# Kernel tuning notes

Hardware: AMD Instinct MI355X
Metric: run time of the kernel (lower is better)

The kernel has to match this reference:

```python
import jax, jax.numpy as jnp
import numpy as np

N_NODES = 50000
N_EDGES = 500000
N_GRAPHS = 64
IN_DIM = 64
HID = 128
N_LAYERS = 2
BN_EPS = 1e-5


def setup_inputs() -> dict:
    key = jax.random.key(0)
    ks = jax.random.split(key, 12)
    x = jax.random.normal(ks[0], (N_NODES, IN_DIM), dtype=jnp.float32)
    edge_index = jax.random.randint(ks[1], (2, N_EDGES), 0, N_NODES, dtype=jnp.int64)
    batch = jnp.sort(jax.random.randint(ks[2], (N_NODES,), 0, N_GRAPHS, dtype=jnp.int64))
    s = 0.05
    W_enc = jax.random.normal(ks[3], (IN_DIM, HID), dtype=jnp.float32) * s
    b_enc = jnp.zeros((HID,), dtype=jnp.float32)
    Wc = jax.random.normal(ks[4], (N_LAYERS, HID, HID), dtype=jnp.float32) * s
    bc = jnp.zeros((N_LAYERS, HID), dtype=jnp.float32)
    gamma = jnp.ones((N_LAYERS, HID), dtype=jnp.float32)
    beta = jnp.zeros((N_LAYERS, HID), dtype=jnp.float32)
    MID = HID // 2
    W1 = jax.random.normal(ks[5], (HID, MID), dtype=jnp.float32) * s
    b1 = jnp.zeros((MID,), dtype=jnp.float32)
    W2 = jax.random.normal(ks[6], (MID, 1), dtype=jnp.float32) * s
    b2 = jnp.zeros((1,), dtype=jnp.float32)
    return {"x": x, "edge_index": edge_index, "batch": batch,
            "W_enc": W_enc, "b_enc": b_enc, "Wc": Wc, "bc": bc,
            "gamma": gamma, "beta": beta, "W1": W1, "b1": b1,
            "W2": W2, "b2": b2}


def _gcn_conv(h, src, dst, norm, W, b, n_nodes):
    # h: [N, HID]; src/dst: [E+N] (self-loops included); norm: [E+N]
    h = h @ W                                   # [N, HID]
    msg = h[src] * norm[:, None]                # gather + normalize
    out = jax.ops.segment_sum(msg, dst, num_segments=n_nodes)  # scatter-add
    return out + b


def _batch_norm(h, g, b):
    mu = jnp.mean(h, axis=0)
    var = jnp.var(h, axis=0)
    return (h - mu) * jax.lax.rsqrt(var + BN_EPS) * g + b


def reference(x, edge_index, batch, W_enc, b_enc, Wc, bc, gamma, beta, W1, b1, W2, b2):
    n = x.shape[0]
    loop = jnp.arange(n, dtype=edge_index.dtype)
    src = jnp.concatenate([edge_index[0], loop])   # [E+N]
    dst = jnp.concatenate([edge_index[1], loop])
    # symmetric GCN normalization with self-loops: deg over target index
    deg = jax.ops.segment_sum(jnp.ones_like(dst, dtype=x.dtype), dst, num_segments=n)
    dinv = jax.lax.rsqrt(deg)                      # deg >= 1 due to self-loops
    norm = dinv[src] * dinv[dst]                   # [E+N]

    h = x @ W_enc + b_enc                          # node encoder
    for l in range(Wc.shape[0]):
        h = _gcn_conv(h, src, dst, norm, Wc[l], bc[l], n)
        h = _batch_norm(h, gamma[l], beta[l])
        h = jax.nn.relu(h)                         # dropout inactive (eval)

    # global mean pool over graphs
    pooled = jax.ops.segment_sum(h, batch, num_segments=N_GRAPHS)
    counts = jax.ops.segment_sum(jnp.ones((n,), dtype=h.dtype), batch, num_segments=N_GRAPHS)
    pooled = pooled / jnp.maximum(counts, 1.0)[:, None]

    z = jax.nn.relu(pooled @ W1 + b1)
    out = jax.nn.sigmoid(z @ W2 + b2)              # [B, 1]
    return out.squeeze(-1)                          # [B]
```

## Files before the change

kernel.cpp:

```cpp
#include <hip/hip_runtime.h>
#include <hip/hip_bf16.h>
#include <hip/hip_fp16.h>
#include <math.h>


typedef _Float16 f16x8 __attribute__((ext_vector_type(8)));
typedef float f32x4 __attribute__((ext_vector_type(4)));

__device__ inline unsigned pack2(float a, float b) {
  union { __half2 h; unsigned u; } p;
  p.h = __floats2half2_rn(a, b);
  return p.u;
}
__device__ inline float2 unpack2(unsigned u) {
  union { unsigned u; __half2 h; } p;
  p.u = u;
  return __half22float2(p.h);
}

__global__ __launch_bounds__(256) void k_setup(
    int* __restrict__ deg, float* __restrict__ pooled,
    float* __restrict__ bnstat, int statTotal, int N, int nbN,
    const float* __restrict__ W_enc, const float* __restrict__ b_enc,
    const float* __restrict__ Wc, unsigned short* __restrict__ MT,
    float* __restrict__ bfold, int NL,
    const float* __restrict__ Wc1, unsigned short* __restrict__ WT1,
    const int* __restrict__ batch, int* __restrict__ gstart) {
  int b = blockIdx.x;
  if (b < nbN) {
    int i = b * 256 + threadIdx.x;
    if (i < N) deg[i] = 1;
    if (i < 64 * 128) pooled[i] = 0.f;
    if (i < statTotal) bnstat[i] = 0.f;
    return;
  }
  b -= nbN;
  if (b < 65) {
    if (threadIdx.x < 128) {
      int n = threadIdx.x;
      int k = b;
      const float* arow = (k < 64) ? (W_enc + (size_t)k * 128) : b_enc;
      float acc = 0.f;
      for (int j = 0; j < 128; j++)
        acc = fmaf(arow[j], Wc[(size_t)j * 128 + n], acc);
      if (k < 64) ((__half*)MT)[(size_t)n * 64 + k] = __float2half(acc);
      else bfold[n] = acc;
    }
    return;
  }
  b -= 65;
  if (b < 64) {
    if (NL > 1) {
      int i = b * 256 + threadIdx.x;
      int n = i & 127, k = i >> 7;
      ((__half*)WT1)[(size_t)n * 128 + k] = __float2half(Wc1[i]);
    }
    return;
  }
  int g = threadIdx.x;
  if (g <= 64) {
    int lo = 0, hi = N;
    while (lo < hi) {
      int mid = (lo + hi) >> 1;
      if (batch[mid] < g) lo = mid + 1;
      else hi = mid;
    }
    gstart[g] = lo;
  }
}

__global__ __launch_bounds__(256) void k_deg(const int* __restrict__ ei, int E,
                                             int* __restrict__ deg) {
  int i = blockIdx.x * 256 + threadIdx.x;
  if (i < E) atomicAdd(&deg[ei[E + i]], 1);
}

__global__ __launch_bounds__(256) void k_scan_a(const int* __restrict__ deg, int N,
                                                int* __restrict__ rowptr,
                                                int* __restrict__ blksum) {
  __shared__ int s[256];
  int t = threadIdx.x;
  int i = blockIdx.x * 256 + t;
  int v = (i < N) ? deg[i] : 0;
  s[t] = v;
  __syncthreads();
  for (int off = 1; off < 256; off <<= 1) {
    int x = (t >= off) ? s[t - off] : 0;
    __syncthreads();
    s[t] += x;
    __syncthreads();
  }
  if (i < N) rowptr[i] = s[t] - v;
  if (t == 255) blksum[blockIdx.x] = s[255];
}

__global__ __launch_bounds__(256) void k_scan_b(int* __restrict__ blksum, int nb) {
  __shared__ int s[256];
  int t = threadIdx.x;
  int v = (t < nb) ? blksum[t] : 0;
  s[t] = v;
  __syncthreads();
  for (int off = 1; off < 256; off <<= 1) {
    int x = (t >= off) ? s[t - off] : 0;
    __syncthreads();
    s[t] += x;
    __syncthreads();
  }
  if (t < nb) blksum[t] = s[t] - v;
}

__global__ __launch_bounds__(256) void k_scan_c(const int* __restrict__ deg, int N,
                                                int total,
                                                const int* __restrict__ blksum,
                                                int* __restrict__ rowptr,
                                                int* __restrict__ cursor,
                                                float* __restrict__ dinv) {
  int i = blockIdx.x * 256 + threadIdx.x;
  if (i < N) {
    int rp = rowptr[i] + blksum[blockIdx.x];
    rowptr[i] = rp;
    cursor[i] = rp;
    dinv[i] = rsqrtf((float)deg[i]);
  } else if (i == N) {
    rowptr[N] = total;
  }
}

__global__ __launch_bounds__(256) void k_fillprep(
    const int* __restrict__ ei, int E, int N, int nbEN,
    int* __restrict__ cursor, int* __restrict__ colx,
    const float* __restrict__ x, const float* __restrict__ dinv,
    unsigned* __restrict__ xs2) {
  int b = blockIdx.x;
  if (b < nbEN) {
    int i = b * 256 + threadIdx.x;
    if (i < E) {
      int s = ei[i];
      int d = ei[E + i];
      int pos = atomicAdd(&cursor[d], 1);
      colx[pos] = s;
    } else if (i < E + N) {
      int j = i - E;
      int pos = atomicAdd(&cursor[j], 1);
      colx[pos] = j;
    }
    return;
  }
  b -= nbEN;
  int i = b * 256 + threadIdx.x;
  if (i < N * 16) {
    int row = i >> 4;
    float4 v = ((const float4*)x)[i];
    float d = dinv[row];
    uint2 o;
    o.x = pack2(v.x * d, v.y * d);
    o.y = pack2(v.z * d, v.w * d);
    ((uint2*)xs2)[i] = o;
  }
}

__global__ __launch_bounds__(256) void k_prep1(const unsigned short* __restrict__ H16,
                                               const float* __restrict__ stat,
                                               const float* __restrict__ gamma,
                                               const float* __restrict__ beta,
                                               float invN,
                                               const float* __restrict__ dinv,
                                               unsigned* __restrict__ hs2,
                                               int total ) {
  __shared__ float scsh[256];
  if (threadIdx.x < 128) {
    int c = threadIdx.x;
    float ss = 0.f, qs = 0.f;
#pragma unroll
    for (int r = 0; r < 8; r++) {
      ss += stat[r * 256 + c];
      qs += stat[r * 256 + 128 + c];
    }
    float mu = ss * invN;
    float var = qs * invN - mu * mu;
    float sc = rsqrtf(var + 1e-5f) * gamma[c];
    scsh[c] = sc;
    scsh[128 + c] = beta[c] - mu * sc;
  }
  __syncthreads();
  int i = blockIdx.x * 256 + threadIdx.x;
  if (i < total) {
    int row = i >> 5;
    int c4 = i & 31;
    uint2 hv = ((const uint2*)H16)[i];
    float2 h01 = unpack2(hv.x), h23 = unpack2(hv.y);
    float4 sc = *(const float4*)&scsh[c4 * 4];
    float4 sh = *(const float4*)&scsh[128 + c4 * 4];
    float d = dinv[row];
    float a = fmaxf(fmaf(h01.x, sc.x, sh.x), 0.f) * d;
    float b = fmaxf(fmaf(h01.y, sc.y, sh.y), 0.f) * d;
    float c = fmaxf(fmaf(h23.x, sc.z, sh.z), 0.f) * d;
    float e = fmaxf(fmaf(h23.y, sc.w, sh.w), 0.f) * d;
    uint2 o;
    o.x = pack2(a, b);
    o.y = pack2(c, e);
    ((uint2*)hs2)[i] = o;
  }
}

__global__ __launch_bounds__(256) void k_agg0(const uint2* __restrict__ xs,
                                              const int* __restrict__ rowptr,
                                              const int* __restrict__ colx,
                                              const float* __restrict__ dinv,
                                              uint2* __restrict__ axh,
                                              float* __restrict__ w, int N) {
  int lane = threadIdx.x & 63;
  int wv = threadIdx.x >> 6;
  int grp = lane >> 4;
  int l16 = lane & 15;
  int wid = blockIdx.x * 4 + wv;
  int nw = gridDim.x * 4;

  for (int base = 4 * wid; base < N; base += 4 * nw) {
    int i = base + grp;
    if (i < N) {
      int beg = rowptr[i];
      int end = rowptr[i + 1];
      float s0 = 0.f, s1 = 0.f, s2 = 0.f, s3 = 0.f, sd = 0.f;
      int e = beg;
#pragma unroll 1
      for (; e + 4 <= end; e += 4) {
        int i0 = colx[e + 0], i1 = colx[e + 1], i2 = colx[e + 2], i3 = colx[e + 3];
        uint2 v0 = xs[(size_t)i0 * 16 + l16];
        uint2 v1 = xs[(size_t)i1 * 16 + l16];
        uint2 v2 = xs[(size_t)i2 * 16 + l16];
        uint2 v3 = xs[(size_t)i3 * 16 + l16];
        float d0 = dinv[i0], d1 = dinv[i1], d2 = dinv[i2], d3 = dinv[i3];
        float2 a0 = unpack2(v0.x), b0 = unpack2(v0.y);
        float2 a1 = unpack2(v1.x), b1 = unpack2(v1.y);
        float2 a2 = unpack2(v2.x), b2 = unpack2(v2.y);
        float2 a3 = unpack2(v3.x), b3 = unpack2(v3.y);
        s0 += (a0.x + a1.x) + (a2.x + a3.x);
        s1 += (a0.y + a1.y) + (a2.y + a3.y);
        s2 += (b0.x + b1.x) + (b2.x + b3.x);
        s3 += (b0.y + b1.y) + (b2.y + b3.y);
        sd += (d0 + d1) + (d2 + d3);
      }
#pragma unroll 1
      for (; e < end; e++) {
        int sr = colx[e];
        uint2 v = xs[(size_t)sr * 16 + l16];
        float2 a = unpack2(v.x), b = unpack2(v.y);
        s0 += a.x; s1 += a.y; s2 += b.x; s3 += b.y;
        sd += dinv[sr];
      }
      float di = dinv[i];
      axh[(size_t)i * 16 + l16] =
          make_uint2(pack2(s0 * di, s1 * di), pack2(s2 * di, s3 * di));
      if (l16 == 0) w[i] = di * sd;
    }
  }
}

__global__ __launch_bounds__(256) void k_agg1(const uint2* __restrict__ hs,
                                              const int* __restrict__ rowptr,
                                              const int* __restrict__ colx,
                                              const float* __restrict__ dinv,
                                              uint2* __restrict__ a1h, int N) {
  int lane = threadIdx.x & 63;
  int wv = threadIdx.x >> 6;
  int half = lane >> 5;
  int l32 = lane & 31;
  int wid = blockIdx.x * 4 + wv;
  int nw = gridDim.x * 4;

  for (int base = 2 * wid; base < N; base += 2 * nw) {
    int i = base + half;
    if (i < N) {
      int beg = rowptr[i];
      int end = rowptr[i + 1];
      float4 s = make_float4(0.f, 0.f, 0.f, 0.f);
      int e = beg;
#pragma unroll 1
      for (; e + 4 <= end; e += 4) {
        int i0 = colx[e + 0], i1 = colx[e + 1], i2 = colx[e + 2], i3 = colx[e + 3];
        uint2 v0 = hs[(size_t)i0 * 32 + l32];
        uint2 v1 = hs[(size_t)i1 * 32 + l32];
        uint2 v2 = hs[(size_t)i2 * 32 + l32];
        uint2 v3 = hs[(size_t)i3 * 32 + l32];
        float2 a0 = unpack2(v0.x), b0 = unpack2(v0.y);
        float2 a1f = unpack2(v1.x), b1f = unpack2(v1.y);
        float2 a2 = unpack2(v2.x), b2 = unpack2(v2.y);
        float2 a3 = unpack2(v3.x), b3 = unpack2(v3.y);
        s.x += (a0.x + a1f.x) + (a2.x + a3.x);
        s.y += (a0.y + a1f.y) + (a2.y + a3.y);
        s.z += (b0.x + b1f.x) + (b2.x + b3.x);
        s.w += (b0.y + b1f.y) + (b2.y + b3.y);
      }
#pragma unroll 1
      for (; e < end; e++) {
        int sr = colx[e];
        uint2 v = hs[(size_t)sr * 32 + l32];
        float2 a = unpack2(v.x), b = unpack2(v.y);
        s.x += a.x; s.y += a.y; s.z += b.x; s.w += b.y;
      }
      float di = dinv[i];
      a1h[(size_t)i * 32 + l32] =
          make_uint2(pack2(s.x * di, s.y * di), pack2(s.z * di, s.w * di));
    }
  }
}

__global__ __launch_bounds__(256) void k_wprep(const float* __restrict__ Wsrc,
                                               unsigned short* __restrict__ WT) {
  int i = blockIdx.x * 256 + threadIdx.x;
  int n = i & 127, k = i >> 7;
  ((__half*)WT)[(size_t)n * 128 + k] = __float2half(Wsrc[i]);
}

template <int K>
__global__ __launch_bounds__(256, 2) void k_gemm_f16(
    const unsigned short* __restrict__ Xh,
    const unsigned short* __restrict__ WT,
    const float* __restrict__ bias,
    const float* __restrict__ wvec,
    const float* __restrict__ bias2,
    float* __restrict__ stat,
    unsigned short* __restrict__ Yh,
    int N) {
  constexpr int KP = K + 8;
  constexpr int K8 = K / 8;
  __shared__ unsigned short Wl[128 * KP];
  __shared__ float red[4][2][128];

  for (int i = threadIdx.x; i < 128 * K8; i += 256) {
    int r = i / K8, c = i - r * K8;
    *(uint4*)&Wl[r * KP + c * 8] = ((const uint4*)(WT + (size_t)r * K))[c];
  }
  __syncthreads();

  int lane = threadIdx.x & 63;
  int wv = threadIdx.x >> 6;
  int l15 = lane & 15;
  int kg = lane >> 4;
  int tileRow = blockIdx.x * 64 + wv * 16;

  int arow = tileRow + l15;
  if (arow >= N) arow = N - 1;
  const unsigned short* xp = Xh + (size_t)arow * K + kg * 8;
  f16x8 af[K / 32];
#pragma unroll
  for (int j = 0; j < K / 32; j++) af[j] = *(const f16x8*)(xp + j * 32);

  f32x4 acc[8];
#pragma unroll
  for (int t = 0; t < 8; t++) acc[t] = {0.f, 0.f, 0.f, 0.f};

  const unsigned short* wb = &Wl[l15 * KP + kg * 8];
#pragma unroll
  for (int j = 0; j < K / 32; j++) {
#pragma unroll
    for (int t = 0; t < 8; t++) {
      f16x8 bf = *(const f16x8*)(wb + t * 16 * KP + j * 32);
      acc[t] = __builtin_amdgcn_mfma_f32_16x16x32_f16(af[j], bf, acc[t], 0, 0, 0);
    }
  }

  int rbase = tileRow + kg * 4;
  float wrow[4];
#pragma unroll
  for (int r = 0; r < 4; r++)
    wrow[r] = (wvec && rbase + r < N) ? wvec[rbase + r] : 0.f;

#pragma unroll
  for (int t = 0; t < 8; t++) {
    int ch = t * 16 + l15;
    float bb = bias[ch];
    float b2v = bias2 ? bias2[ch] : 0.f;
    float s = 0.f, q = 0.f;
#pragma unroll
    for (int r = 0; r < 4; r++) {
      int row = rbase + r;
      if (row < N) {
        float o = acc[t][r] + bb;
        if (wvec) o = fmaf(wrow[r], b2v, o);
        __half oh = __float2half(o);
        Yh[(size_t)row * 128 + ch] = *(unsigned short*)&oh;
        s += o;
        q += o * o;
      }
    }
    s += __shfl_xor(s, 16); s += __shfl_xor(s, 32);
    q += __shfl_xor(q, 16); q += __shfl_xor(q, 32);
    if (kg == 0) { red[wv][0][ch] = s; red[wv][1][ch] = q; }
  }
  __syncthreads();
  int st = threadIdx.x >> 7, ch2 = threadIdx.x & 127;
  float v = red[0][st][ch2] + red[1][st][ch2] + red[2][st][ch2] + red[3][st][ch2];
  atomicAdd(&stat[(blockIdx.x & 7) * 256 + st * 128 + ch2], v);
}

__global__ __launch_bounds__(128) void k_pool(const unsigned short* __restrict__ H16,
                                              const float* __restrict__ stat,
                                              const float* __restrict__ gamma,
                                              const float* __restrict__ beta,
                                              float invN,
                                              const int* __restrict__ gstart,
                                              float* __restrict__ pooled) {
  int c = threadIdx.x;
  float ss = 0.f, qs = 0.f;
#pragma unroll
  for (int r = 0; r < 8; r++) {
    ss += stat[r * 256 + c];
    qs += stat[r * 256 + 128 + c];
  }
  float mu = ss * invN;
  float var = qs * invN - mu * mu;
  float sc = rsqrtf(var + 1e-5f) * gamma[c];
  float sh = beta[c] - mu * sc;

  int g = blockIdx.x >> 3;
  int part = blockIdx.x & 7;
  int beg = gstart[g], end = gstart[g + 1];
  int len = end - beg;
  int pbeg = beg + (len * part) / 8;
  int pend = beg + (len * (part + 1)) / 8;
  float s = 0.f;
  for (int r = pbeg; r < pend; r++) {
    float v = __half2float(((const __half*)H16)[(size_t)r * 128 + c]);
    s += fmaxf(fmaf(v, sc, sh), 0.f);
  }
  atomicAdd(&pooled[g * 128 + c], s);
}

__global__ __launch_bounds__(256) void k_mlp(const float* __restrict__ pooled,
                                             const int* __restrict__ gstart,
                                             const float* __restrict__ W1,
                                             const float* __restrict__ b1,
                                             const float* __restrict__ W2,
                                             const float* __restrict__ b2,
                                             float* __restrict__ out) {
  __shared__ float P[64 * 128];
  __shared__ float Z[64 * 64];
  for (int i = threadIdx.x; i < 64 * 128; i += 256) {
    int g = i >> 7;
    int cnt = gstart[g + 1] - gstart[g];
    P[i] = pooled[i] / (float)(cnt > 1 ? cnt : 1);
  }
  __syncthreads();
  for (int i = threadIdx.x; i < 64 * 64; i += 256) {
    int g = i >> 6, m = i & 63;
    float acc = b1[m];
    for (int k = 0; k < 128; k++) acc += P[(g << 7) + k] * W1[k * 64 + m];
    Z[i] = fmaxf(acc, 0.f);
  }
  __syncthreads();
  if (threadIdx.x < 64) {
    int g = threadIdx.x;
    float acc = b2[0];
    for (int m = 0; m < 64; m++) acc += Z[(g << 6) + m] * W2[m];
    out[g] = 1.f / (1.f + expf(-acc));
  }
}


extern "C" void kernel_launch(void* const* d_in, const int* in_sizes, int n_in,
                              void* d_out, int out_size, void* d_ws, size_t ws_size,
                              hipStream_t stream) {
  const float* x      = (const float*)d_in[0];
  const int*   ei     = (const int*)d_in[1];
  const int*   batch  = (const int*)d_in[2];
  const float* W_enc  = (const float*)d_in[3];
  const float* b_enc  = (const float*)d_in[4];
  const float* Wc     = (const float*)d_in[5];
  const float* bc     = (const float*)d_in[6];
  const float* gamma  = (const float*)d_in[7];
  const float* beta   = (const float*)d_in[8];
  const float* W1     = (const float*)d_in[9];
  const float* b1     = (const float*)d_in[10];
  const float* W2     = (const float*)d_in[11];
  const float* b2     = (const float*)d_in[12];
  float* out = (float*)d_out;

  const int N = in_sizes[2];
  const int E = in_sizes[1] / 2;
  const int NL = in_sizes[6] / 128;

  size_t off = 0;
  auto alloc = [&](size_t bytes) {
    void* p = (char*)d_ws + off;
    off += (bytes + 255) & ~(size_t)255;
    return p;
  };
  unsigned short* h16 = (unsigned short*)alloc((size_t)N * 128 * 2);
  int*   deg    = (int*)alloc((size_t)N * 4);
  float* dinv   = (float*)alloc((size_t)N * 4);
  int*   rowptr = (int*)alloc((size_t)(N + 1) * 4);
  int*   cursor = (int*)alloc((size_t)N * 4);
  int*   colx   = (int*)alloc((size_t)(E + N) * 4);
  int*   blksum = (int*)alloc(1024 * 4);
  float* bnstat = (float*)alloc((size_t)NL * 2048 * 4);
  float* pooled = (float*)alloc(64 * 128 * 4);
  int*   gstart = (int*)alloc(65 * 4);
  unsigned short* MT  = (unsigned short*)alloc(128 * 64 * 2);
  unsigned short* WT1 = (unsigned short*)alloc(128 * 128 * 2);
  float* bfold  = (float*)alloc(128 * 4);
  unsigned* xs  = (unsigned*)alloc((size_t)N * 64 * 2);
  unsigned* hs  = (unsigned*)alloc((size_t)N * 128 * 2);
  unsigned* axh = (unsigned*)alloc((size_t)N * 64 * 2);
  uint2*    a1h = (uint2*)alloc((size_t)N * 128 * 2);
  float* wv     = (float*)alloc((size_t)N * 4);

  int nbN = (N + 255) / 256;
  int nbEN = (E + N + 255) / 256;
  float invN = 1.f / (float)N;

  k_setup<<<nbN + 130, 256, 0, stream>>>(
      deg, pooled, bnstat, NL * 2048, N, nbN, W_enc, b_enc, Wc, MT, bfold, NL,
      Wc + (size_t)128 * 128, WT1, batch, gstart);
  k_deg<<<(E + 255) / 256, 256, 0, stream>>>(ei, E, deg);
  k_scan_a<<<nbN, 256, 0, stream>>>(deg, N, rowptr, blksum);
  k_scan_b<<<1, 256, 0, stream>>>(blksum, nbN);
  k_scan_c<<<(N + 1 + 255) / 256, 256, 0, stream>>>(deg, N, E + N, blksum,
                                                    rowptr, cursor, dinv);
  k_fillprep<<<nbEN + (N * 16 + 255) / 256, 256, 0, stream>>>(
      ei, E, N, nbEN, cursor, colx, x, dinv, xs);

  int tiles = (N + 63) / 64;

  k_agg0<<<2048, 256, 0, stream>>>((const uint2*)xs, rowptr, colx, dinv,
                                   (uint2*)axh, wv, N);
  k_gemm_f16<64><<<tiles, 256, 0, stream>>>(
      (const unsigned short*)axh, MT, bc, wv, bfold, bnstat, h16, N);

  for (int l = 1; l < NL; l++) {
    if (l > 1)
      k_wprep<<<64, 256, 0, stream>>>(Wc + (size_t)l * 128 * 128, WT1);
    k_prep1<<<(N * 32 + 255) / 256, 256, 0, stream>>>(
        h16, bnstat + (l - 1) * 2048, gamma + (l - 1) * 128,
        beta + (l - 1) * 128, invN, dinv, hs, N * 32);
    k_agg1<<<2048, 256, 0, stream>>>((const uint2*)hs, rowptr, colx, dinv,
                                     a1h, N);
    k_gemm_f16<128><<<tiles, 256, 0, stream>>>(
        (const unsigned short*)a1h, WT1, bc + l * 128, nullptr, nullptr,
        bnstat + l * 2048, h16, N);
  }

  k_pool<<<64 * 8, 128, 0, stream>>>(h16, bnstat + (NL - 1) * 2048,
                                     gamma + (NL - 1) * 128,
                                     beta + (NL - 1) * 128, invN, gstart,
                                     pooled);
  k_mlp<<<1, 256, 0, stream>>>(pooled, gstart, W1, b1, W2, b2, out);
}
```

Baseline: 278.0 us.

## Fuse aggregation with GEMM, fold BN-apply into gather, merge pool and MLP

Each GCN layer's sparse aggregation now runs inside the MFMA GEMM kernel, one 64-row tile per block, with the aggregated rows staged in shared memory instead of written out and read back. The previous layer's batch-norm, ReLU and dinv scaling are applied on the fly while gathering neighbors, which removes the separate prep pass over the hidden activations. The block-sum scan kernel is replaced by each block reducing the earlier block sums itself, and pooling plus the MLP become one kernel per graph, so several launches and atomics go away. In exchange, the BN/ReLU math is recomputed once per edge instead of once per node, the grid shrinks to one block per tile with more shared memory per block, and the weight tile is read from global memory rather than LDS.

```diff
diff --git a/kernel.cpp b/kernel.cpp
--- a/kernel.cpp
+++ b/kernel.cpp
@@ -19,8 +19,8 @@
 }
 
 __global__ __launch_bounds__(256) void k_setup(
-    int* __restrict__ deg, float* __restrict__ pooled,
-    float* __restrict__ bnstat, int statTotal, int N, int nbN,
+    int* __restrict__ deg, float* __restrict__ bnstat, int statTotal,
+    int N, int nbN,
     const float* __restrict__ W_enc, const float* __restrict__ b_enc,
     const float* __restrict__ Wc, unsigned short* __restrict__ MT,
     float* __restrict__ bfold, int NL,
@@ -30,7 +30,6 @@
   if (b < nbN) {
     int i = b * 256 + threadIdx.x;
     if (i < N) deg[i] = 1;
-    if (i < 64 * 128) pooled[i] = 0.f;
     if (i < statTotal) bnstat[i] = 0.f;
     return;
   }
@@ -94,30 +93,26 @@
   if (t == 255) blksum[blockIdx.x] = s[255];
 }
 
-__global__ __launch_bounds__(256) void k_scan_b(int* __restrict__ blksum, int nb) {
-  __shared__ int s[256];
-  int t = threadIdx.x;
-  int v = (t < nb) ? blksum[t] : 0;
-  s[t] = v;
-  __syncthreads();
-  for (int off = 1; off < 256; off <<= 1) {
-    int x = (t >= off) ? s[t - off] : 0;
-    __syncthreads();
-    s[t] += x;
-    __syncthreads();
-  }
-  if (t < nb) blksum[t] = s[t] - v;
-}
-
 __global__ __launch_bounds__(256) void k_scan_c(const int* __restrict__ deg, int N,
                                                 int total,
                                                 const int* __restrict__ blksum,
                                                 int* __restrict__ rowptr,
                                                 int* __restrict__ cursor,
                                                 float* __restrict__ dinv) {
-  int i = blockIdx.x * 256 + threadIdx.x;
+  __shared__ int red[256];
+  int t = threadIdx.x, b = blockIdx.x;
+  int acc = 0;
+  for (int j = t; j < b; j += 256) acc += blksum[j];
+  red[t] = acc;
+  __syncthreads();
+  for (int off = 128; off > 0; off >>= 1) {
+    if (t < off) red[t] += red[t + off];
+    __syncthreads();
+  }
+  int prefix = red[0];
+  int i = b * 256 + t;
   if (i < N) {
-    int rp = rowptr[i] + blksum[blockIdx.x];
+    int rp = rowptr[i] + prefix;
     rowptr[i] = rp;
     cursor[i] = rp;
     dinv[i] = rsqrtf((float)deg[i]);
@@ -159,22 +154,137 @@
   }
 }
 
-__global__ __launch_bounds__(256) void k_prep1(const unsigned short* __restrict__ H16,
-                                               const float* __restrict__ stat,
-                                               const float* __restrict__ gamma,
-                                               const float* __restrict__ beta,
-                                               float invN,
-                                               const float* __restrict__ dinv,
-                                               unsigned* __restrict__ hs2,
-                                               int total ) {
+__global__ __launch_bounds__(256, 2) void k_aggemm0(
+    const uint2* __restrict__ xs, const int* __restrict__ rowptr,
+    const int* __restrict__ colx, const float* __restrict__ dinv,
+    const unsigned short* __restrict__ MT,
+    const float* __restrict__ bias,
+    const float* __restrict__ bias2,
+    float* __restrict__ stat,
+    unsigned short* __restrict__ Yh, int N) {
+  constexpr int KP = 68;
+  __shared__ unsigned short Al[64 * KP];
+  __shared__ float wvl[64];
+  __shared__ float red[4][2][128];
+
+  int lane = threadIdx.x & 63;
+  int wv = threadIdx.x >> 6;
+  int grp = lane >> 4, l16 = lane & 15;
+  int rowBlk = blockIdx.x * 64;
+
+#pragma unroll 1
+  for (int it = 0; it < 4; it++) {
+    int lr = it * 16 + wv * 4 + grp;
+    int i = rowBlk + lr;
+    float s0 = 0.f, s1 = 0.f, s2 = 0.f, s3 = 0.f, sd = 0.f;
+    if (i < N) {
+      int beg = rowptr[i], end = rowptr[i + 1];
+      int e = beg;
+#pragma unroll 1
+      for (; e + 8 <= end; e += 8) {
+        int ix[8];
+#pragma unroll
+        for (int u = 0; u < 8; u++) ix[u] = colx[e + u];
+        uint2 v[8];
+        float dd[8];
+#pragma unroll
+        for (int u = 0; u < 8; u++) { v[u] = xs[(size_t)ix[u] * 16 + l16]; dd[u] = dinv[ix[u]]; }
+#pragma unroll
+        for (int u = 0; u < 8; u++) {
+          float2 a = unpack2(v[u].x), b = unpack2(v[u].y);
+          s0 += a.x; s1 += a.y; s2 += b.x; s3 += b.y;
+          sd += dd[u];
+        }
+      }
+#pragma unroll 1
+      for (; e < end; e++) {
+        int sr = colx[e];
+        uint2 vv = xs[(size_t)sr * 16 + l16];
+        float2 a = unpack2(vv.x), b = unpack2(vv.y);
+        s0 += a.x; s1 += a.y; s2 += b.x; s3 += b.y;
+        sd += dinv[sr];
+      }
+    }
+    float di = (i < N) ? dinv[i] : 0.f;
+    *(uint2*)&Al[lr * KP + l16 * 4] =
+        make_uint2(pack2(s0 * di, s1 * di), pack2(s2 * di, s3 * di));
+    if (l16 == 0) wvl[lr] = di * sd;
+  }
+  __syncthreads();
+
+  int l15 = lane & 15;
+  int kg = lane >> 4;
+  f16x8 af[2];
+#pragma unroll
+  for (int j = 0; j < 2; j++)
+    af[j] = *(const f16x8*)&Al[(wv * 16 + l15) * KP + kg * 8 + j * 32];
+
+  f32x4 acc[8];
+#pragma unroll
+  for (int t = 0; t < 8; t++) acc[t] = {0.f, 0.f, 0.f, 0.f};
+#pragma unroll
+  for (int j = 0; j < 2; j++) {
+#pragma unroll
+    for (int t = 0; t < 8; t++) {
+      f16x8 bf = *(const f16x8*)&MT[(size_t)(t * 16 + l15) * 64 + kg * 8 + j * 32];
+      acc[t] = __builtin_amdgcn_mfma_f32_16x16x32_f16(af[j], bf, acc[t], 0, 0, 0);
+    }
+  }
+
+  int rbaseL = wv * 16 + kg * 4;
+  int rbase = rowBlk + rbaseL;
+  float wrow[4];
+#pragma unroll
+  for (int r = 0; r < 4; r++) wrow[r] = wvl[rbaseL + r];
+
+#pragma unroll
+  for (int t = 0; t < 8; t++) {
+    int ch = t * 16 + l15;
+    float bb = bias[ch];
+    float b2v = bias2[ch];
+    float s = 0.f, q = 0.f;
+#pragma unroll
+    for (int r = 0; r < 4; r++) {
+      int row = rbase + r;
+      if (row < N) {
+        float o = fmaf(wrow[r], b2v, acc[t][r] + bb);
+        __half oh = __float2half(o);
+        Yh[(size_t)row * 128 + ch] = *(unsigned short*)&oh;
+        s += o;
+        q += o * o;
+      }
+    }
+    s += __shfl_xor(s, 16); s += __shfl_xor(s, 32);
+    q += __shfl_xor(q, 16); q += __shfl_xor(q, 32);
+    if (kg == 0) { red[wv][0][ch] = s; red[wv][1][ch] = q; }
+  }
+  __syncthreads();
+  int st = threadIdx.x >> 7, ch2 = threadIdx.x & 127;
+  float v = red[0][st][ch2] + red[1][st][ch2] + red[2][st][ch2] + red[3][st][ch2];
+  atomicAdd(&stat[(blockIdx.x & 7) * 256 + st * 128 + ch2], v);
+}
+
+__global__ __launch_bounds__(256, 2) void k_aggemm1(
+    const unsigned short* __restrict__ Hprev,
+    const int* __restrict__ rowptr, const int* __restrict__ colx,
+    const float* __restrict__ dinv,
+    const unsigned short* __restrict__ WT,
+    const float* __restrict__ statPrev, const float* __restrict__ gamma,
+    const float* __restrict__ beta, float invN,
+    const float* __restrict__ bias,
+    float* __restrict__ statCur, unsigned short* __restrict__ Yh, int N) {
+  constexpr int KP = 136;
+  __shared__ unsigned short Al[64 * KP];
   __shared__ float scsh[256];
+  __shared__ float red[4][2][128];
+
   if (threadIdx.x < 128) {
     int c = threadIdx.x;
     float ss = 0.f, qs = 0.f;
 #pragma unroll
     for (int r = 0; r < 8; r++) {
-      ss += stat[r * 256 + c];
-      qs += stat[r * 256 + 128 + c];
+      ss += statPrev[r * 256 + c];
+      qs += statPrev[r * 256 + 128 + c];
     }
     float mu = ss * invN;
     float var = qs * invN - mu * mu;
@@ -183,127 +293,115 @@
     scsh[128 + c] = beta[c] - mu * sc;
   }
   __syncthreads();
-  int i = blockIdx.x * 256 + threadIdx.x;
-  if (i < total) {
-    int row = i >> 5;
-    int c4 = i & 31;
-    uint2 hv = ((const uint2*)H16)[i];
-    float2 h01 = unpack2(hv.x), h23 = unpack2(hv.y);
-    float4 sc = *(const float4*)&scsh[c4 * 4];
-    float4 sh = *(const float4*)&scsh[128 + c4 * 4];
-    float d = dinv[row];
-    float a = fmaxf(fmaf(h01.x, sc.x, sh.x), 0.f) * d;
-    float b = fmaxf(fmaf(h01.y, sc.y, sh.y), 0.f) * d;
-    float c = fmaxf(fmaf(h23.x, sc.z, sh.z), 0.f) * d;
-    float e = fmaxf(fmaf(h23.y, sc.w, sh.w), 0.f) * d;
-    uint2 o;
-    o.x = pack2(a, b);
-    o.y = pack2(c, e);
-    ((uint2*)hs2)[i] = o;
-  }
-}
-
-__global__ __launch_bounds__(256) void k_agg0(const uint2* __restrict__ xs,
-                                              const int* __restrict__ rowptr,
-                                              const int* __restrict__ colx,
-                                              const float* __restrict__ dinv,
-                                              uint2* __restrict__ axh,
-                                              float* __restrict__ w, int N) {
+
   int lane = threadIdx.x & 63;
   int wv = threadIdx.x >> 6;
-  int grp = lane >> 4;
-  int l16 = lane & 15;
-  int wid = blockIdx.x * 4 + wv;
-  int nw = gridDim.x * 4;
-
-  for (int base = 4 * wid; base < N; base += 4 * nw) {
-    int i = base + grp;
+  int half = lane >> 5, l32 = lane & 31;
+  int rowBlk = blockIdx.x * 64;
+  const uint2* Hp = (const uint2*)Hprev;
+  float4 sc = ((const float4*)scsh)[l32];
+  float4 sh = ((const float4*)(scsh + 128))[l32];
+
+#pragma unroll 1
+  for (int it = 0; it < 8; it++) {
+    int lr = it * 8 + wv * 2 + half;
+    int i = rowBlk + lr;
+    float4 s = make_float4(0.f, 0.f, 0.f, 0.f);
     if (i < N) {
-      int beg = rowptr[i];
-      int end = rowptr[i + 1];
-      float s0 = 0.f, s1 = 0.f, s2 = 0.f, s3 = 0.f, sd = 0.f;
+      int beg = rowptr[i], end = rowptr[i + 1];
       int e = beg;
 #pragma unroll 1
       for (; e + 4 <= end; e += 4) {
         int i0 = colx[e + 0], i1 = colx[e + 1], i2 = colx[e + 2], i3 = colx[e + 3];
-        uint2 v0 = xs[(size_t)i0 * 16 + l16];
-        uint2 v1 = xs[(size_t)i1 * 16 + l16];
-        uint2 v2 = xs[(size_t)i2 * 16 + l16];
-        uint2 v3 = xs[(size_t)i3 * 16 + l16];
+        uint2 v0 = Hp[(size_t)i0 * 32 + l32];
+        uint2 v1 = Hp[(size_t)i1 * 32 + l32];
+        uint2 v2 = Hp[(size_t)i2 * 32 + l32];
+        uint2 v3 = Hp[(size_t)i3 * 32 + l32];
         float d0 = dinv[i0], d1 = dinv[i1], d2 = dinv[i2], d3 = dinv[i3];
-        float2 a0 = unpack2(v0.x), b0 = unpack2(v0.y);
-        float2 a1 = unpack2(v1.x), b1 = unpack2(v1.y);
-        float2 a2 = unpack2(v2.x), b2 = unpack2(v2.y);
-        float2 a3 = unpack2(v3.x), b3 = unpack2(v3.y);
-        s0 += (a0.x + a1.x) + (a2.x + a3.x);
-        s1 += (a0.y + a1.y) + (a2.y + a3.y);
-        s2 += (b0.x + b1.x) + (b2.x + b3.x);
-        s3 += (b0.y + b1.y) + (b2.y + b3.y);
-        sd += (d0 + d1) + (d2 + d3);
+        float2 a, b;
+        a = unpack2(v0.x); b = unpack2(v0.y);
+        s.x += fmaxf(fmaf(a.x, sc.x, sh.x), 0.f) * d0;
+        s.y += fmaxf(fmaf(a.y, sc.y, sh.y), 0.f) * d0;
+        s.z += fmaxf(fmaf(b.x, sc.z, sh.z), 0.f) * d0;
+        s.w += fmaxf(fmaf(b.y, sc.w, sh.w), 0.f) * d0;
+        a = unpack2(v1.x); b = unpack2(v1.y);
+        s.x += fmaxf(fmaf(a.x, sc.x, sh.x), 0.f) * d1;
+        s.y += fmaxf(fmaf(a.y, sc.y, sh.y), 0.f) * d1;
+        s.z += fmaxf(fmaf(b.x, sc.z, sh.z), 0.f) * d1;
+        s.w += fmaxf(fmaf(b.y, sc.w, sh.w), 0.f) * d1;
+        a = unpack2(v2.x); b = unpack2(v2.y);
+        s.x += fmaxf(fmaf(a.x, sc.x, sh.x), 0.f) * d2;
+        s.y += fmaxf(fmaf(a.y, sc.y, sh.y), 0.f) * d2;
+        s.z += fmaxf(fmaf(b.x, sc.z, sh.z), 0.f) * d2;
+        s.w += fmaxf(fmaf(b.y, sc.w, sh.w), 0.f) * d2;
+        a = unpack2(v3.x); b = unpack2(v3.y);
+        s.x += fmaxf(fmaf(a.x, sc.x, sh.x), 0.f) * d3;
+        s.y += fmaxf(fmaf(a.y, sc.y, sh.y), 0.f) * d3;
+        s.z += fmaxf(fmaf(b.x, sc.z, sh.z), 0.f) * d3;
+        s.w += fmaxf(fmaf(b.y, sc.w, sh.w), 0.f) * d3;
       }
 #pragma unroll 1
       for (; e < end; e++) {
         int sr = colx[e];
-        uint2 v = xs[(size_t)sr * 16 + l16];
-        float2 a = unpack2(v.x), b = unpack2(v.y);
-        s0 += a.x; s1 += a.y; s2 += b.x; s3 += b.y;
-        sd += dinv[sr];
+        uint2 vv = Hp[(size_t)sr * 32 + l32];
+        float dsr = dinv[sr];
+        float2 a = unpack2(vv.x), b = unpack2(vv.y);
+        s.x += fmaxf(fmaf(a.x, sc.x, sh.x), 0.f) * dsr;
+        s.y += fmaxf(fmaf(a.y, sc.y, sh.y), 0.f) * dsr;
+        s.z += fmaxf(fmaf(b.x, sc.z, sh.z), 0.f) * dsr;
+        s.w += fmaxf(fmaf(b.y, sc.w, sh.w), 0.f) * dsr;
       }
-      float di = dinv[i];
-      axh[(size_t)i * 16 + l16] =
-          make_uint2(pack2(s0 * di, s1 * di), pack2(s2 * di, s3 * di));
-      if (l16 == 0) w[i] = di * sd;
-    }
-  }
-}
-
-__global__ __launch_bounds__(256) void k_agg1(const uint2* __restrict__ hs,
-                                              const int* __restrict__ rowptr,
-                                              const int* __restrict__ colx,
-                                              const float* __restrict__ dinv,
-                                              uint2* __restrict__ a1h, int N) {
-  int lane = threadIdx.x & 63;
-  int wv = threadIdx.x >> 6;
-  int half = lane >> 5;
-  int l32 = lane & 31;
-  int wid = blockIdx.x * 4 + wv;
-  int nw = gridDim.x * 4;
-
-  for (int base = 2 * wid; base < N; base += 2 * nw) {
-    int i = base + half;
-    if (i < N) {
-      int beg = rowptr[i];
-      int end = rowptr[i + 1];
-      float4 s = make_float4(0.f, 0.f, 0.f, 0.f);
-      int e = beg;
-#pragma unroll 1
-      for (; e + 4 <= end; e += 4) {
-        int i0 = colx[e + 0], i1 = colx[e + 1], i2 = colx[e + 2], i3 = colx[e + 3];
-        uint2 v0 = hs[(size_t)i0 * 32 + l32];
-        uint2 v1 = hs[(size_t)i1 * 32 + l32];
-        uint2 v2 = hs[(size_t)i2 * 32 + l32];
-        uint2 v3 = hs[(size_t)i3 * 32 + l32];
-        float2 a0 = unpack2(v0.x), b0 = unpack2(v0.y);
-        float2 a1f = unpack2(v1.x), b1f = unpack2(v1.y);
-        float2 a2 = unpack2(v2.x), b2 = unpack2(v2.y);
-        float2 a3 = unpack2(v3.x), b3 = unpack2(v3.y);
-        s.x += (a0.x + a1f.x) + (a2.x + a3.x);
-        s.y += (a0.y + a1f.y) + (a2.y + a3.y);
-        s.z += (b0.x + b1f.x) + (b2.x + b3.x);
-        s.w += (b0.y + b1f.y) + (b2.y + b3.y);
+    }
+    float di = (i < N) ? dinv[i] : 0.f;
+    *(uint2*)&Al[lr * KP + l32 * 4] =
+        make_uint2(pack2(s.x * di, s.y * di), pack2(s.z * di, s.w * di));
+  }
+  __syncthreads();
+
+  int l15 = lane & 15;
+  int kg = lane >> 4;
+  f16x8 af[4];
+#pragma unroll
+  for (int j = 0; j < 4; j++)
+    af[j] = *(const f16x8*)&Al[(wv * 16 + l15) * KP + kg * 8 + j * 32];
+
+  f32x4 acc[8];
+#pragma unroll
+  for (int t = 0; t < 8; t++) acc[t] = {0.f, 0.f, 0.f, 0.f};
+#pragma unroll
+  for (int j = 0; j < 4; j++) {
+#pragma unroll
+    for (int t = 0; t < 8; t++) {
+      f16x8 bf = *(const f16x8*)&WT[(size_t)(t * 16 + l15) * 128 + kg * 8 + j * 32];
+      acc[t] = __builtin_amdgcn_mfma_f32_16x16x32_f16(af[j], bf, acc[t], 0, 0, 0);
+    }
+  }
+
+  int rbase = rowBlk + wv * 16 + kg * 4;
+#pragma unroll
+  for (int t = 0; t < 8; t++) {
+    int ch = t * 16 + l15;
+    float bb = bias[ch];
+    float s = 0.f, q = 0.f;
+#pragma unroll
+    for (int r = 0; r < 4; r++) {
+      int row = rbase + r;
+      if (row < N) {
+        float o = acc[t][r] + bb;
+        __half oh = __float2half(o);
+        Yh[(size_t)row * 128 + ch] = *(unsigned short*)&oh;
+        s += o;
+        q += o * o;
       }
-#pragma unroll 1
-      for (; e < end; e++) {
-        int sr = colx[e];
-        uint2 v = hs[(size_t)sr * 32 + l32];
-        float2 a = unpack2(v.x), b = unpack2(v.y);
-        s.x += a.x; s.y += a.y; s.z += b.x; s.w += b.y;
-      }
-      float di = dinv[i];
-      a1h[(size_t)i * 32 + l32] =
-          make_uint2(pack2(s.x * di, s.y * di), pack2(s.z * di, s.w * di));
-    }
-  }
+    }
+    s += __shfl_xor(s, 16); s += __shfl_xor(s, 32);
+    q += __shfl_xor(q, 16); q += __shfl_xor(q, 32);
+    if (kg == 0) { red[wv][0][ch] = s; red[wv][1][ch] = q; }
+  }
+  __syncthreads();
+  int st = threadIdx.x >> 7, ch2 = threadIdx.x & 127;
+  float v = red[0][st][ch2] + red[1][st][ch2] + red[2][st][ch2] + red[3][st][ch2];
+  atomicAdd(&statCur[(blockIdx.x & 7) * 256 + st * 128 + ch2], v);
 }
 
 __global__ __launch_bounds__(256) void k_wprep(const float* __restrict__ Wsrc,
@@ -313,148 +411,62 @@
   ((__half*)WT)[(size_t)n * 128 + k] = __float2half(Wsrc[i]);
 }
 
-template <int K>
-__global__ __launch_bounds__(256, 2) void k_gemm_f16(
-    const unsigned short* __restrict__ Xh,
-    const unsigned short* __restrict__ WT,
-    const float* __restrict__ bias,
-    const float* __restrict__ wvec,
-    const float* __restrict__ bias2,
-    float* __restrict__ stat,
-    unsigned short* __restrict__ Yh,
-    int N) {
-  constexpr int KP = K + 8;
-  constexpr int K8 = K / 8;
-  __shared__ unsigned short Wl[128 * KP];
-  __shared__ float red[4][2][128];
-
-  for (int i = threadIdx.x; i < 128 * K8; i += 256) {
-    int r = i / K8, c = i - r * K8;
-    *(uint4*)&Wl[r * KP + c * 8] = ((const uint4*)(WT + (size_t)r * K))[c];
-  }
-  __syncthreads();
-
-  int lane = threadIdx.x & 63;
-  int wv = threadIdx.x >> 6;
-  int l15 = lane & 15;
-  int kg = lane >> 4;
-  int tileRow = blockIdx.x * 64 + wv * 16;
-
-  int arow = tileRow + l15;
-  if (arow >= N) arow = N - 1;
-  const unsigned short* xp = Xh + (size_t)arow * K + kg * 8;
-  f16x8 af[K / 32];
-#pragma unroll
-  for (int j = 0; j < K / 32; j++) af[j] = *(const f16x8*)(xp + j * 32);
-
-  f32x4 acc[8];
-#pragma unroll
-  for (int t = 0; t < 8; t++) acc[t] = {0.f, 0.f, 0.f, 0.f};
-
-  const unsigned short* wb = &Wl[l15 * KP + kg * 8];
-#pragma unroll
-  for (int j = 0; j < K / 32; j++) {
-#pragma unroll
-    for (int t = 0; t < 8; t++) {
-      f16x8 bf = *(const f16x8*)(wb + t * 16 * KP + j * 32);
-      acc[t] = __builtin_amdgcn_mfma_f32_16x16x32_f16(af[j], bf, acc[t], 0, 0, 0);
-    }
-  }
-
-  int rbase = tileRow + kg * 4;
-  float wrow[4];
-#pragma unroll
-  for (int r = 0; r < 4; r++)
-    wrow[r] = (wvec && rbase + r < N) ? wvec[rbase + r] : 0.f;
-
-#pragma unroll
-  for (int t = 0; t < 8; t++) {
-    int ch = t * 16 + l15;
-    float bb = bias[ch];
-    float b2v = bias2 ? bias2[ch] : 0.f;
-    float s = 0.f, q = 0.f;
-#pragma unroll
-    for (int r = 0; r < 4; r++) {
-      int row = rbase + r;
-      if (row < N) {
-        float o = acc[t][r] + bb;
-        if (wvec) o = fmaf(wrow[r], b2v, o);
-        __half oh = __float2half(o);
-        Yh[(size_t)row * 128 + ch] = *(unsigned short*)&oh;
-        s += o;
-        q += o * o;
-      }
-    }
-    s += __shfl_xor(s, 16); s += __shfl_xor(s, 32);
-    q += __shfl_xor(q, 16); q += __shfl_xor(q, 32);
-    if (kg == 0) { red[wv][0][ch] = s; red[wv][1][ch] = q; }
-  }
-  __syncthreads();
-  int st = threadIdx.x >> 7, ch2 = threadIdx.x & 127;
-  float v = red[0][st][ch2] + red[1][st][ch2] + red[2][st][ch2] + red[3][st][ch2];
-  atomicAdd(&stat[(blockIdx.x & 7) * 256 + st * 128 + ch2], v);
-}
-
-__global__ __launch_bounds__(128) void k_pool(const unsigned short* __restrict__ H16,
-                                              const float* __restrict__ stat,
-                                              const float* __restrict__ gamma,
-                                              const float* __restrict__ beta,
-                                              float invN,
-                                              const int* __restrict__ gstart,
-                                              float* __restrict__ pooled) {
-  int c = threadIdx.x;
-  float ss = 0.f, qs = 0.f;
-#pragma unroll
-  for (int r = 0; r < 8; r++) {
-    ss += stat[r * 256 + c];
-    qs += stat[r * 256 + 128 + c];
-  }
-  float mu = ss * invN;
-  float var = qs * invN - mu * mu;
-  float sc = rsqrtf(var + 1e-5f) * gamma[c];
-  float sh = beta[c] - mu * sc;
-
-  int g = blockIdx.x >> 3;
-  int part = blockIdx.x & 7;
+__global__ __launch_bounds__(256) void k_poolmlp(
+    const unsigned short* __restrict__ H16, const float* __restrict__ stat,
+    const float* __restrict__ gamma, const float* __restrict__ beta, float invN,
+    const int* __restrict__ gstart,
+    const float* __restrict__ W1, const float* __restrict__ b1,
+    const float* __restrict__ W2, const float* __restrict__ b2,
+    float* __restrict__ out) {
+  __shared__ float scsh[256];
+  __shared__ float psum[256];
+  __shared__ float P[128];
+  __shared__ float z[64];
+  if (threadIdx.x < 128) {
+    int c = threadIdx.x;
+    float ss = 0.f, qs = 0.f;
+#pragma unroll
+    for (int r = 0; r < 8; r++) {
+      ss += stat[r * 256 + c];
+      qs += stat[r * 256 + 128 + c];
+    }
+    float mu = ss * invN;
+    float var = qs * invN - mu * mu;
+    float sc = rsqrtf(var + 1e-5f) * gamma[c];
+    scsh[c] = sc;
+    scsh[128 + c] = beta[c] - mu * sc;
+  }
+  __syncthreads();
+
+  int g = blockIdx.x;
   int beg = gstart[g], end = gstart[g + 1];
   int len = end - beg;
-  int pbeg = beg + (len * part) / 8;
-  int pend = beg + (len * (part + 1)) / 8;
+  int split = threadIdx.x >> 7, ch = threadIdx.x & 127;
+  float sc = scsh[ch], sh = scsh[128 + ch];
+  int r0 = beg + (len * split) / 2;
+  int r1 = beg + (len * (split + 1)) / 2;
   float s = 0.f;
-  for (int r = pbeg; r < pend; r++) {
-    float v = __half2float(((const __half*)H16)[(size_t)r * 128 + c]);
+  for (int r = r0; r < r1; r++) {
+    float v = __half2float(((const __half*)H16)[(size_t)r * 128 + ch]);
     s += fmaxf(fmaf(v, sc, sh), 0.f);
   }
-  atomicAdd(&pooled[g * 128 + c], s);
-}
-
-__global__ __launch_bounds__(256) void k_mlp(const float* __restrict__ pooled,
-                                             const int* __restrict__ gstart,
-                                             const float* __restrict__ W1,
-                                             const float* __restrict__ b1,
-                                             const float* __restrict__ W2,
-                                             const float* __restrict__ b2,
-                                             float* __restrict__ out) {
-  __shared__ float P[64 * 128];
-  __shared__ float Z[64 * 64];
-  for (int i = threadIdx.x; i < 64 * 128; i += 256) {
-    int g = i >> 7;
-    int cnt = gstart[g + 1] - gstart[g];
-    P[i] = pooled[i] / (float)(cnt > 1 ? cnt : 1);
-  }
-  __syncthreads();
-  for (int i = threadIdx.x; i < 64 * 64; i += 256) {
-    int g = i >> 6, m = i & 63;
-    float acc = b1[m];
-    for (int k = 0; k < 128; k++) acc += P[(g << 7) + k] * W1[k * 64 + m];
-    Z[i] = fmaxf(acc, 0.f);
-  }
+  psum[threadIdx.x] = s;
+  __syncthreads();
+  if (threadIdx.x < 128)
+    P[threadIdx.x] =
+        (psum[threadIdx.x] + psum[threadIdx.x + 128]) / (float)(len > 1 ? len : 1);
   __syncthreads();
   if (threadIdx.x < 64) {
-    int g = threadIdx.x;
-    float acc = b2[0];
-    for (int m = 0; m < 64; m++) acc += Z[(g << 6) + m] * W2[m];
-    out[g] = 1.f / (1.f + expf(-acc));
+    int m = threadIdx.x;
+    float a = b1[m];
+    for (int k = 0; k < 128; k++) a = fmaf(P[k], W1[k * 64 + m], a);
+    z[m] = fmaxf(a, 0.f);
+  }
+  __syncthreads();
+  if (threadIdx.x == 0) {
+    float a = b2[0];
+    for (int m = 0; m < 64; m++) a = fmaf(z[m], W2[m], a);
+    out[g] = 1.f / (1.f + expf(-a));
   }
 }
 
@@ -487,7 +499,8 @@
     off += (bytes + 255) & ~(size_t)255;
     return p;
   };
-  unsigned short* h16 = (unsigned short*)alloc((size_t)N * 128 * 2);
+  unsigned short* h16a = (unsigned short*)alloc((size_t)N * 128 * 2);
+  unsigned short* h16b = (unsigned short*)alloc((size_t)N * 128 * 2);
   int*   deg    = (int*)alloc((size_t)N * 4);
   float* dinv   = (float*)alloc((size_t)N * 4);
   int*   rowptr = (int*)alloc((size_t)(N + 1) * 4);
@@ -495,55 +508,43 @@
   int*   colx   = (int*)alloc((size_t)(E + N) * 4);
   int*   blksum = (int*)alloc(1024 * 4);
   float* bnstat = (float*)alloc((size_t)NL * 2048 * 4);
-  float* pooled = (float*)alloc(64 * 128 * 4);
   int*   gstart = (int*)alloc(65 * 4);
   unsigned short* MT  = (unsigned short*)alloc(128 * 64 * 2);
   unsigned short* WT1 = (unsigned short*)alloc(128 * 128 * 2);
   float* bfold  = (float*)alloc(128 * 4);
   unsigned* xs  = (unsigned*)alloc((size_t)N * 64 * 2);
-  unsigned* hs  = (unsigned*)alloc((size_t)N * 128 * 2);
-  unsigned* axh = (unsigned*)alloc((size_t)N * 64 * 2);
-  uint2*    a1h = (uint2*)alloc((size_t)N * 128 * 2);
-  float* wv     = (float*)alloc((size_t)N * 4);
 
   int nbN = (N + 255) / 256;
   int nbEN = (E + N + 255) / 256;
   float invN = 1.f / (float)N;
+  int tiles = (N + 63) / 64;
 
   k_setup<<<nbN + 130, 256, 0, stream>>>(
-      deg, pooled, bnstat, NL * 2048, N, nbN, W_enc, b_enc, Wc, MT, bfold, NL,
+      deg, bnstat, NL * 2048, N, nbN, W_enc, b_enc, Wc, MT, bfold, NL,
       Wc + (size_t)128 * 128, WT1, batch, gstart);
   k_deg<<<(E + 255) / 256, 256, 0, stream>>>(ei, E, deg);
   k_scan_a<<<nbN, 256, 0, stream>>>(deg, N, rowptr, blksum);
-  k_scan_b<<<1, 256, 0, stream>>>(blksum, nbN);
-  k_scan_c<<<(N + 1 + 255) / 256, 256, 0, stream>>>(deg, N, E + N, blksum,
-                                                    rowptr, cursor, dinv);
+  k_scan_c<<<nbN, 256, 0, stream>>>(deg, N, E + N, blksum, rowptr, cursor, dinv);
   k_fillprep<<<nbEN + (N * 16 + 255) / 256, 256, 0, stream>>>(
       ei, E, N, nbEN, cursor, colx, x, dinv, xs);
 
-  int tiles = (N + 63) / 64;
-
-  k_agg0<<<2048, 256, 0, stream>>>((const uint2*)xs, rowptr, colx, dinv,
-                                   (uint2*)axh, wv, N);
-  k_gemm_f16<64><<<tiles, 256, 0, stream>>>(
-      (const unsigned short*)axh, MT, bc, wv, bfold, bnstat, h16, N);
-
+  k_aggemm0<<<tiles, 256, 0, stream>>>((const uint2*)xs, rowptr, colx, dinv,
+                                       MT, bc, bfold, bnstat, h16a, N);
+
+  unsigned short* cur = h16a;
+  unsigned short* nxt = h16b;
   for (int l = 1; l < NL; l++) {
     if (l > 1)
       k_wprep<<<64, 256, 0, stream>>>(Wc + (size_t)l * 128 * 128, WT1);
-    k_prep1<<<(N * 32 + 255) / 256, 256, 0, stream>>>(
-        h16, bnstat + (l - 1) * 2048, gamma + (l - 1) * 128,
-        beta + (l - 1) * 128, invN, dinv, hs, N * 32);
-    k_agg1<<<2048, 256, 0, stream>>>((const uint2*)hs, rowptr, colx, dinv,
-                                     a1h, N);
-    k_gemm_f16<128><<<tiles, 256, 0, stream>>>(
-        (const unsigned short*)a1h, WT1, bc + l * 128, nullptr, nullptr,
-        bnstat + l * 2048, h16, N);
-  }
-
-  k_pool<<<64 * 8, 128, 0, stream>>>(h16, bnstat + (NL - 1) * 2048,
-                                     gamma + (NL - 1) * 128,
-                                     beta + (NL - 1) * 128, invN, gstart,
-                                     pooled);
-  k_mlp<<<1, 256, 0, stream>>>(pooled, gstart, W1, b1, W2, b2, out);
-}
+    k_aggemm1<<<tiles, 256, 0, stream>>>(
+        cur, rowptr, colx, dinv, WT1, bnstat + (l - 1) * 2048,
+        gamma + (l - 1) * 128, beta + (l - 1) * 128, invN, bc + l * 128,
+        bnstat + l * 2048, nxt, N);
+    unsigned short* tmp = cur; cur = nxt; nxt = tmp;
+  }
+
+  k_poolmlp<<<64, 256, 0, stream>>>(cur, bnstat + (NL - 1) * 2048,
+                                    gamma + (NL - 1) * 128,
+                                    beta + (NL - 1) * 128, invN, gstart,
+                                    W1, b1, W2, b2, out);
+}
```

Result: slower. 359.2 us (+29.2%).
